# Performance work log

Measured on AMD Instinct MI355X. Metric: run time of the kernel, lower is better.

Reference implementation:

```python
import jax, jax.numpy as jnp
import numpy as np

B, N, K = 8, 512, 16            # batches, proposals per batch, knn neighbors
C_POOL = 256                    # pooled feature dim (hardcoded 256 in source)
G_MLP = [128, 128]              # GLOBAL_INFORMATION.MLP_LAYERS
IN_DIM = C_POOL + G_MLP[-1]     # gnn_input_dim = 384
LAYERS = [512, 512, 512]


def _xavier(key, shape):
    fan_out, fan_in = shape
    lim = np.sqrt(6.0 / (fan_in + fan_out))
    return jax.random.uniform(key, shape, jnp.float32, -lim, lim)


def setup_inputs() -> dict:
    key = jax.random.key(0)
    ks = jax.random.split(key, 12)
    rois = jax.random.normal(ks[0], (B, N, 7), jnp.float32)
    rois = rois.at[:, :, :3].multiply(20.0)  # spread box centers spatially
    pooled_features = jax.random.normal(ks[1], (B, N, C_POOL), jnp.float32)

    # knn_graph per batch (loop=False): edges (neighbor j -> center i)
    coords = rois[:, :, :3]
    d2 = jnp.sum((coords[:, :, None, :] - coords[:, None, :, :]) ** 2, -1)  # [B,N,N]
    d2 = d2 + jnp.eye(N, dtype=jnp.float32) * 1e9                           # no self loops
    _, nbr = jax.lax.top_k(-d2, K)                                          # [B,N,K]
    offs = (jnp.arange(B) * N)[:, None, None]
    src = (nbr + offs).reshape(-1)
    dst = (jnp.broadcast_to(jnp.arange(N)[None, :, None], (B, N, K)) + offs).reshape(-1)
    edge_index = jnp.stack([src, dst]).astype(jnp.int32)                    # [2, B*N*K]

    # global-information MLP params: Linear(7,128), Linear(128,128)
    gW1 = _xavier(ks[2], (G_MLP[0], 7)); gb1 = jnp.zeros((G_MLP[0],), jnp.float32)
    gW2 = _xavier(ks[3], (G_MLP[1], G_MLP[0])); gb2 = jnp.zeros((G_MLP[1],), jnp.float32)

    # EdgeConv fc params: in = 2*in_dim of layer
    fcW1 = _xavier(ks[4], (LAYERS[0], 2 * IN_DIM)); fcb1 = jnp.zeros((LAYERS[0],), jnp.float32)
    fcW2 = _xavier(ks[5], (LAYERS[1], 2 * LAYERS[0])); fcb2 = jnp.zeros((LAYERS[1],), jnp.float32)
    fcW3 = _xavier(ks[6], (LAYERS[2], 2 * LAYERS[1])); fcb3 = jnp.zeros((LAYERS[2],), jnp.float32)

    return dict(rois=rois, pooled_features=pooled_features, edge_index=edge_index,
                gW1=gW1, gb1=gb1, gW2=gW2, gb2=gb2,
                fcW1=fcW1, fcb1=fcb1, fcW2=fcW2, fcb2=fcb2, fcW3=fcW3, fcb3=fcb3)


def reference(rois, pooled_features, edge_index,
              gW1, gb1, gW2, gb2,
              fcW1, fcb1, fcW2, fcb2, fcW3, fcb3):
    # global information MLP on proposal boxes
    g = jax.nn.relu(rois @ gW1.T + gb1)
    g = jax.nn.relu(g @ gW2.T + gb2)                      # [B,N,128]
    x = jnp.concatenate([pooled_features, g], -1).reshape(-1, IN_DIM)  # [B*N, 384]

    src, dst = edge_index[0], edge_index[1]
    n_nodes = B * N
    feats = [x]
    for W, b in ((fcW1, fcb1), (fcW2, fcb2), (fcW3, fcb3)):
        x_i = x[dst]                                      # target features [E,d]
        x_j = x[src]                                      # source features [E,d]
        msg = jax.nn.relu(jnp.concatenate([x_j - x_i, x_i], -1) @ W.T + b)  # [E,out]
        x = jax.ops.segment_max(msg, dst, num_segments=n_nodes)  # scatter-max aggr
        feats.append(x)
    return jnp.concatenate(feats, -1)                     # [B*N, 384+512*3]
```

## Files before the change

kernel.cpp:

```cpp
#include <hip/hip_runtime.h>
#include <hip/hip_bf16.h>

#define BN_NODES 4096
#define KNN 16
#define C_POOL 256
#define G_DIM 128
#define IN_DIM 384
#define L_DIM 512
#define OUT_STRIDE 1920

#define X1_OFF 384
#define X2_OFF 896
#define X3_OFF 1408

typedef __attribute__((ext_vector_type(8))) __bf16 bf16x8;
typedef __attribute__((ext_vector_type(4))) float floatx4;
typedef __attribute__((ext_vector_type(8))) unsigned short ushortx8;

static __device__ __forceinline__ ushort f2bf(float v) {
  return __builtin_bit_cast(ushort, __float2bfloat16(v));
}
static __device__ __forceinline__ float bf2f(ushort u) {
  return __builtin_bit_cast(float, ((unsigned)u) << 16);
}
static __device__ __forceinline__ void gld_lds(const ushort* g, ushort* l) {
  __builtin_amdgcn_global_load_lds(
      (const __attribute__((address_space(1))) void*)g,
      (__attribute__((address_space(3))) void*)l, 16, 0, 0);
}

__global__ __launch_bounds__(256) void prep_kernel(
    const float* __restrict__ rois, const float* __restrict__ pooled,
    const float* __restrict__ gW1, const float* __restrict__ gb1,
    const float* __restrict__ gW2, const float* __restrict__ gb2,
    const float* __restrict__ W0, const float* __restrict__ W1,
    const float* __restrict__ W2, float* __restrict__ out,
    ushort* __restrict__ Xb0, ushort* __restrict__ Wb0,
    ushort* __restrict__ Wb1, ushort* __restrict__ Wb2) {
  const int t = threadIdx.x;
  if (blockIdx.x >= 512) {
    int wi = blockIdx.x - 512;
    const float* W;
    ushort* Wb;
    int K, base;
    if (wi < 384) {
      W = W0; Wb = Wb0; K = IN_DIM; base = wi;
    } else if (wi < 896) {
      W = W1; Wb = Wb1; K = L_DIM; base = wi - 384;
    } else {
      W = W2; Wb = Wb2; K = L_DIM; base = wi - 896;
    }
    int elem = base * 1024 + t * 4;
    int j = elem / K;
    int k = elem - j * K;
    const float* srcp = (j < 512) ? W + (size_t)j * (2 * K) + k
                                  : W + (size_t)(j - 512) * (2 * K) + K + k;
    ushort4 pk;
    pk.x = f2bf(srcp[0]);
    pk.y = f2bf(srcp[1]);
    pk.z = f2bf(srcp[2]);
    pk.w = f2bf(srcp[3]);
    *(ushort4*)(Wb + (size_t)j * K + k) = pk;
    return;
  }
  const int nb = blockIdx.x * 8;
  const int c = t & 127;
  const int nh = t >> 7;
  __shared__ float rs[8 * 7];
  __shared__ __align__(16) float h1[8][G_DIM];
  if (t < 56) rs[t] = rois[(size_t)nb * 7 + t];
  __syncthreads();
  {
    float w1[7];
#pragma unroll
    for (int i = 0; i < 7; i++) w1[i] = gW1[c * 7 + i];
    float b1 = gb1[c];
#pragma unroll
    for (int n = nh * 4; n < nh * 4 + 4; n++) {
      float a = b1;
#pragma unroll
      for (int i = 0; i < 7; i++) a += rs[n * 7 + i] * w1[i];
      h1[n][c] = fmaxf(a, 0.f);
    }
  }
  __syncthreads();
  float acc[4];
  {
    float b2 = gb2[c];
#pragma unroll
    for (int n = 0; n < 4; n++) acc[n] = b2;
    const float4* w4 = (const float4*)(gW2 + (size_t)c * G_DIM);
#pragma unroll 4
    for (int kc = 0; kc < G_DIM / 4; kc++) {
      float4 wv = w4[kc];
#pragma unroll
      for (int n = 0; n < 4; n++) {
        float4 hv = ((const float4*)h1[nh * 4 + n])[kc];
        acc[n] += wv.x * hv.x + wv.y * hv.y + wv.z * hv.z + wv.w * hv.w;
      }
    }
  }
#pragma unroll
  for (int n = 0; n < 4; n++) {
    int node = nb + nh * 4 + n;
    float g = fmaxf(acc[n], 0.f);
    const float* prow = pooled + (size_t)node * C_POOL;
    float p0 = prow[c], p1 = prow[G_DIM + c];
    float* orow = out + (size_t)node * OUT_STRIDE;
    orow[c] = p0;
    orow[G_DIM + c] = p1;
    orow[C_POOL + c] = g;
    ushort* xrow = Xb0 + (size_t)node * IN_DIM;
    xrow[c] = f2bf(p0);
    xrow[G_DIM + c] = f2bf(p1);
    xrow[C_POOL + c] = f2bf(g);
  }
}

template <int K>
__global__ __launch_bounds__(512) void mfma_gemm_kernel(
    const ushort* __restrict__ Xb, const ushort* __restrict__ Wb,
    ushort* __restrict__ PQb) {
  __shared__ __align__(16) ushort sA[2][128 * 64];
  __shared__ __align__(16) ushort sB[2][64 * 64];
  const int tid = threadIdx.x;
  const int lane = tid & 63;
  const int w = tid >> 6;
  const int wm = w >> 1;
  const int wn = w & 1;
  const int fr = lane & 15;
  const int kc = lane >> 4;
  const int bm = blockIdx.x, bn = blockIdx.y;
  constexpr int NT = K / 64;

  const int ta0 = w, ta1 = w + 8;
  const int rt0 = ta0 >> 1, ks0 = ta0 & 1;
  const int rt1 = ta1 >> 1, ks1 = ta1 & 1;
  const int ctB = w >> 1, ksB = w & 1;
  const ushort* gA0 = Xb + (size_t)(bm * 128 + rt0 * 16 + fr) * K + ks0 * 32 + kc * 8;
  const ushort* gA1 = Xb + (size_t)(bm * 128 + rt1 * 16 + fr) * K + ks1 * 32 + kc * 8;
  const ushort* gB = Wb + (size_t)(bn * 64 + ctB * 16 + fr) * K + ksB * 32 + kc * 8;

  floatx4 acc[2][2];
#pragma unroll
  for (int i = 0; i < 2; i++)
#pragma unroll
    for (int j = 0; j < 2; j++) acc[i][j] = (floatx4){0.f, 0.f, 0.f, 0.f};

  gld_lds(gA0, &sA[0][ta0 * 512 + lane * 8]);
  gld_lds(gA1, &sA[0][ta1 * 512 + lane * 8]);
  gld_lds(gB, &sB[0][w * 512 + lane * 8]);
  __syncthreads();

#pragma unroll
  for (int t = 0; t < NT; ++t) {
    const int cur = t & 1;
    if (t + 1 < NT) {
      const int k0n = (t + 1) * 64;
      gld_lds(gA0 + k0n, &sA[cur ^ 1][ta0 * 512 + lane * 8]);
      gld_lds(gA1 + k0n, &sA[cur ^ 1][ta1 * 512 + lane * 8]);
      gld_lds(gB + k0n, &sB[cur ^ 1][w * 512 + lane * 8]);
    }
#pragma unroll
    for (int ks = 0; ks < 2; ks++) {
      bf16x8 af[2], bfr[2];
#pragma unroll
      for (int i = 0; i < 2; i++)
        af[i] =
            *(const bf16x8*)&sA[cur][((wm * 2 + i) * 2 + ks) * 512 + lane * 8];
#pragma unroll
      for (int j = 0; j < 2; j++)
        bfr[j] =
            *(const bf16x8*)&sB[cur][((wn * 2 + j) * 2 + ks) * 512 + lane * 8];
#pragma unroll
      for (int i = 0; i < 2; i++)
#pragma unroll
        for (int j = 0; j < 2; j++)
          acc[i][j] = __builtin_amdgcn_mfma_f32_16x16x32_bf16(af[i], bfr[j],
                                                              acc[i][j], 0, 0,
                                                              0);
    }
    __syncthreads();
  }

  const int rowB = bm * 128 + wm * 32 + kc * 4;
  const int colB = bn * 64 + wn * 32 + fr;
#pragma unroll
  for (int i = 0; i < 2; i++)
#pragma unroll
    for (int j = 0; j < 2; j++)
#pragma unroll
      for (int r = 0; r < 4; r++)
        PQb[(size_t)(rowB + i * 16 + r) * 1024 + colB + j * 16] =
            f2bf(acc[i][j][r]);
}

__global__ __launch_bounds__(512) void edge_kernel(
    const ushort* __restrict__ PQb, const int* __restrict__ src,
    const float* __restrict__ bias, float* __restrict__ out, int out_off,
    ushort* __restrict__ Xb, int write_x) {
  const int bid = blockIdx.x;
  const int n = (bid & 7) * 512 + (bid >> 3) * 8 + (threadIdx.x >> 6);
  const int l = threadIdx.x & 63;

  int nbr[KNN];
  {
    const int4* sp = (const int4*)(src + (size_t)n * KNN);
#pragma unroll
    for (int k4 = 0; k4 < 4; k4++) {
      int4 v = sp[k4];
      nbr[k4 * 4 + 0] = v.x;
      nbr[k4 * 4 + 1] = v.y;
      nbr[k4 * 4 + 2] = v.z;
      nbr[k4 * 4 + 3] = v.w;
    }
  }

  const ushort* own = PQb + (size_t)n * 1024 + l * 8;
  ushortx8 pu = *(const ushortx8*)own;
  ushortx8 qu = *(const ushortx8*)(own + 512);

  float m[8];
#pragma unroll
  for (int c = 0; c < 8; c++) m[c] = -1e30f;
#pragma unroll
  for (int k = 0; k < KNN; k++) {
    ushortx8 u = *(const ushortx8*)(PQb + (size_t)nbr[k] * 1024 + l * 8);
#pragma unroll
    for (int c = 0; c < 8; c++) m[c] = fmaxf(m[c], bf2f(u[c]));
  }

  const float4 bb0 = *(const float4*)&bias[l * 8];
  const float4 bb1 = *(const float4*)&bias[l * 8 + 4];
  float res[8];
#pragma unroll
  for (int c = 0; c < 8; c++) {
    float bbv = (c < 4) ? ((const float*)&bb0)[c] : ((const float*)&bb1)[c - 4];
    res[c] = fmaxf(m[c] - bf2f(pu[c]) + bf2f(qu[c]) + bbv, 0.f);
  }

  float* orow = out + (size_t)n * OUT_STRIDE + out_off + l * 8;
  *(float4*)orow = (float4){res[0], res[1], res[2], res[3]};
  *(float4*)(orow + 4) = (float4){res[4], res[5], res[6], res[7]};
  if (write_x) {
    ushortx8 pk;
#pragma unroll
    for (int c = 0; c < 8; c++) pk[c] = f2bf(res[c]);
    *(ushortx8*)(Xb + (size_t)n * L_DIM + l * 8) = pk;
  }
}

extern "C" void kernel_launch(void* const* d_in, const int* in_sizes, int n_in,
                              void* d_out, int out_size, void* d_ws,
                              size_t ws_size, hipStream_t stream) {
  const float* rois = (const float*)d_in[0];
  const float* pooled = (const float*)d_in[1];
  const int* edge_index = (const int*)d_in[2];
  const float* gW1 = (const float*)d_in[3];
  const float* gb1 = (const float*)d_in[4];
  const float* gW2 = (const float*)d_in[5];
  const float* gb2 = (const float*)d_in[6];
  const float* fcW[3] = {(const float*)d_in[7], (const float*)d_in[9],
                         (const float*)d_in[11]};
  const float* fcb[3] = {(const float*)d_in[8], (const float*)d_in[10],
                         (const float*)d_in[12]};
  float* out = (float*)d_out;
  const int* src = edge_index;

  char* ws = (char*)d_ws;
  ushort* PQb = (ushort*)ws;
  ushort* Xb = (ushort*)(ws + (size_t)8 * 1024 * 1024);
  ushort* Wb[3] = {(ushort*)(ws + (size_t)12 * 1024 * 1024),
                   (ushort*)(ws + (size_t)13 * 1024 * 1024),
                   (ushort*)(ws + (size_t)14 * 1024 * 1024)};

  prep_kernel<<<1920, 256, 0, stream>>>(rois, pooled, gW1, gb1, gW2, gb2,
                                        fcW[0], fcW[1], fcW[2], out, Xb, Wb[0],
                                        Wb[1], Wb[2]);

  mfma_gemm_kernel<IN_DIM><<<dim3(32, 16), 512, 0, stream>>>(Xb, Wb[0], PQb);
  edge_kernel<<<512, 512, 0, stream>>>(PQb, src, fcb[0], out, X1_OFF, Xb, 1);
  mfma_gemm_kernel<L_DIM><<<dim3(32, 16), 512, 0, stream>>>(Xb, Wb[1], PQb);
  edge_kernel<<<512, 512, 0, stream>>>(PQb, src, fcb[1], out, X2_OFF, Xb, 1);
  mfma_gemm_kernel<L_DIM><<<dim3(32, 16), 512, 0, stream>>>(Xb, Wb[2], PQb);
  edge_kernel<<<512, 512, 0, stream>>>(PQb, src, fcb[2], out, X3_OFF, Xb, 0);
}
```

Measured before the change: 167.1 us.

## Defer layer-2/3 weight conversion into edge kernels and stage gW2 in LDS

Weight conversion to bf16 for layers 2 and 3 moves out of the prep kernel and into the edge kernels of the preceding layers, where it runs alongside the aggregation work. This shrinks the prep grid. Prep blocks now each convert four chunks of W0 in a loop. The global-MLP second layer stages gW2 into padded shared memory and reads scalar weights per k instead of per-thread global float4 loads. The cost is extra LDS usage (~66KB) in prep, which may limit occupancy, and extra tail work in the edge kernels.

```diff
diff --git a/kernel.cpp b/kernel.cpp
--- a/kernel.cpp
+++ b/kernel.cpp
@@ -33,41 +33,48 @@
     const float* __restrict__ rois, const float* __restrict__ pooled,
     const float* __restrict__ gW1, const float* __restrict__ gb1,
     const float* __restrict__ gW2, const float* __restrict__ gb2,
-    const float* __restrict__ W0, const float* __restrict__ W1,
-    const float* __restrict__ W2, float* __restrict__ out,
-    ushort* __restrict__ Xb0, ushort* __restrict__ Wb0,
-    ushort* __restrict__ Wb1, ushort* __restrict__ Wb2) {
+    const float* __restrict__ W0, float* __restrict__ out,
+    ushort* __restrict__ Xb0, ushort* __restrict__ Wb0) {
   const int t = threadIdx.x;
   if (blockIdx.x >= 512) {
-    int wi = blockIdx.x - 512;
-    const float* W;
-    ushort* Wb;
-    int K, base;
-    if (wi < 384) {
-      W = W0; Wb = Wb0; K = IN_DIM; base = wi;
-    } else if (wi < 896) {
-      W = W1; Wb = Wb1; K = L_DIM; base = wi - 384;
-    } else {
-      W = W2; Wb = Wb2; K = L_DIM; base = wi - 896;
-    }
-    int elem = base * 1024 + t * 4;
-    int j = elem / K;
-    int k = elem - j * K;
-    const float* srcp = (j < 512) ? W + (size_t)j * (2 * K) + k
-                                  : W + (size_t)(j - 512) * (2 * K) + K + k;
-    ushort4 pk;
-    pk.x = f2bf(srcp[0]);
-    pk.y = f2bf(srcp[1]);
-    pk.z = f2bf(srcp[2]);
-    pk.w = f2bf(srcp[3]);
-    *(ushort4*)(Wb + (size_t)j * K + k) = pk;
+    const int base = (blockIdx.x - 512) * 1024;
+#pragma unroll
+    for (int p = 0; p < 4; ++p) {
+      int g = base + p * 256 + t;
+      int elem = g * 4;
+      int j = elem / IN_DIM;
+      int k = elem - j * IN_DIM;
+      const float* srcp = (j < 512)
+                              ? W0 + (size_t)j * (2 * IN_DIM) + k
+                              : W0 + (size_t)(j - 512) * (2 * IN_DIM) + IN_DIM + k;
+      ushort4 pk;
+      pk.x = f2bf(srcp[0]);
+      pk.y = f2bf(srcp[1]);
+      pk.z = f2bf(srcp[2]);
+      pk.w = f2bf(srcp[3]);
+      *(ushort4*)(Wb0 + (size_t)j * IN_DIM + k) = pk;
+    }
     return;
   }
+  __shared__ float sW2[128 * 129];
+  __shared__ float rs[64];
+  __shared__ __align__(16) float h1[8][G_DIM];
   const int nb = blockIdx.x * 8;
   const int c = t & 127;
   const int nh = t >> 7;
-  __shared__ float rs[8 * 7];
-  __shared__ __align__(16) float h1[8][G_DIM];
+  {
+    const float4* g4 = (const float4*)gW2;
+#pragma unroll
+    for (int p = 0; p < 16; ++p) {
+      int f = p * 256 + t;
+      float4 v = g4[f];
+      float* dst = &sW2[(f >> 5) * 129 + (f & 31) * 4];
+      dst[0] = v.x;
+      dst[1] = v.y;
+      dst[2] = v.z;
+      dst[3] = v.w;
+    }
+  }
   if (t < 56) rs[t] = rois[(size_t)nb * 7 + t];
   __syncthreads();
   {
@@ -89,14 +96,18 @@
     float b2 = gb2[c];
 #pragma unroll
     for (int n = 0; n < 4; n++) acc[n] = b2;
-    const float4* w4 = (const float4*)(gW2 + (size_t)c * G_DIM);
+    const float* wrow = &sW2[c * 129];
 #pragma unroll 4
-    for (int kc = 0; kc < G_DIM / 4; kc++) {
-      float4 wv = w4[kc];
-#pragma unroll
-      for (int n = 0; n < 4; n++) {
-        float4 hv = ((const float4*)h1[nh * 4 + n])[kc];
-        acc[n] += wv.x * hv.x + wv.y * hv.y + wv.z * hv.z + wv.w * hv.w;
+    for (int k4 = 0; k4 < G_DIM / 4; k4++) {
+      float4 hv[4];
+#pragma unroll
+      for (int n = 0; n < 4; n++) hv[n] = ((const float4*)h1[nh * 4 + n])[k4];
+#pragma unroll
+      for (int q = 0; q < 4; q++) {
+        float wv = wrow[k4 * 4 + q];
+#pragma unroll
+        for (int n = 0; n < 4; n++)
+          acc[n] += wv * ((const float*)&hv[n])[q];
       }
     }
   }
@@ -137,9 +148,12 @@
   const int rt0 = ta0 >> 1, ks0 = ta0 & 1;
   const int rt1 = ta1 >> 1, ks1 = ta1 & 1;
   const int ctB = w >> 1, ksB = w & 1;
-  const ushort* gA0 = Xb + (size_t)(bm * 128 + rt0 * 16 + fr) * K + ks0 * 32 + kc * 8;
-  const ushort* gA1 = Xb + (size_t)(bm * 128 + rt1 * 16 + fr) * K + ks1 * 32 + kc * 8;
-  const ushort* gB = Wb + (size_t)(bn * 64 + ctB * 16 + fr) * K + ksB * 32 + kc * 8;
+  const ushort* gA0 =
+      Xb + (size_t)(bm * 128 + rt0 * 16 + fr) * K + ks0 * 32 + kc * 8;
+  const ushort* gA1 =
+      Xb + (size_t)(bm * 128 + rt1 * 16 + fr) * K + ks1 * 32 + kc * 8;
+  const ushort* gB =
+      Wb + (size_t)(bn * 64 + ctB * 16 + fr) * K + ksB * 32 + kc * 8;
 
   floatx4 acc[2][2];
 #pragma unroll
@@ -198,7 +212,8 @@
 __global__ __launch_bounds__(512) void edge_kernel(
     const ushort* __restrict__ PQb, const int* __restrict__ src,
     const float* __restrict__ bias, float* __restrict__ out, int out_off,
-    ushort* __restrict__ Xb, int write_x) {
+    ushort* __restrict__ Xb, int write_x, const float* __restrict__ wsrc,
+    ushort* __restrict__ wdst) {
   const int bid = blockIdx.x;
   const int n = (bid & 7) * 512 + (bid >> 3) * 8 + (threadIdx.x >> 6);
   const int l = threadIdx.x & 63;
@@ -247,6 +262,23 @@
 #pragma unroll
     for (int c = 0; c < 8; c++) pk[c] = f2bf(res[c]);
     *(ushortx8*)(Xb + (size_t)n * L_DIM + l * 8) = pk;
+  }
+
+  if (wsrc != nullptr) {
+    int g = bid * 512 + threadIdx.x;
+    if (g < 131072) {
+      int elem = g * 4;
+      int j = elem >> 9;
+      int k = elem & 511;
+      const float* srcp = (j < 512) ? wsrc + ((size_t)j << 10) + k
+                                    : wsrc + ((size_t)(j - 512) << 10) + 512 + k;
+      ushort4 pk;
+      pk.x = f2bf(srcp[0]);
+      pk.y = f2bf(srcp[1]);
+      pk.z = f2bf(srcp[2]);
+      pk.w = f2bf(srcp[3]);
+      *(ushort4*)(wdst + ((size_t)j << 9) + k) = pk;
+    }
   }
 }
 
@@ -274,14 +306,16 @@
                    (ushort*)(ws + (size_t)13 * 1024 * 1024),
                    (ushort*)(ws + (size_t)14 * 1024 * 1024)};
 
-  prep_kernel<<<1920, 256, 0, stream>>>(rois, pooled, gW1, gb1, gW2, gb2,
-                                        fcW[0], fcW[1], fcW[2], out, Xb, Wb[0],
-                                        Wb[1], Wb[2]);
+  prep_kernel<<<608, 256, 0, stream>>>(rois, pooled, gW1, gb1, gW2, gb2,
+                                       fcW[0], out, Xb, Wb[0]);
 
   mfma_gemm_kernel<IN_DIM><<<dim3(32, 16), 512, 0, stream>>>(Xb, Wb[0], PQb);
-  edge_kernel<<<512, 512, 0, stream>>>(PQb, src, fcb[0], out, X1_OFF, Xb, 1);
+  edge_kernel<<<512, 512, 0, stream>>>(PQb, src, fcb[0], out, X1_OFF, Xb, 1,
+                                       fcW[1], Wb[1]);
   mfma_gemm_kernel<L_DIM><<<dim3(32, 16), 512, 0, stream>>>(Xb, Wb[1], PQb);
-  edge_kernel<<<512, 512, 0, stream>>>(PQb, src, fcb[1], out, X2_OFF, Xb, 1);
+  edge_kernel<<<512, 512, 0, stream>>>(PQb, src, fcb[1], out, X2_OFF, Xb, 1,
+                                       fcW[2], Wb[2]);
   mfma_gemm_kernel<L_DIM><<<dim3(32, 16), 512, 0, stream>>>(Xb, Wb[2], PQb);
-  edge_kernel<<<512, 512, 0, stream>>>(PQb, src, fcb[2], out, X3_OFF, Xb, 0);
-}
+  edge_kernel<<<512, 512, 0, stream>>>(PQb, src, fcb[2], out, X3_OFF, Xb, 0,
+                                       nullptr, nullptr);
+}
```

Result: no change. 166.4 us (median of 2 runs) (-0.4%).
